# Performance work log

Hardware: AMD Instinct MI355X
Metric: run time of the kernel (lower is better)

The kernel has to match this reference:

```python
import jax, jax.numpy as jnp
import numpy as np

B, T, LA, L = 4, 32, 32, 512
D, H, C = 2048, 16, 128
KV_DIM = 2048
K = T * LA  # total kv tokens per batch element
EPS = 1e-5


def _ln(x):
    m = jnp.mean(x, axis=-1, keepdims=True)
    v = jnp.var(x, axis=-1, keepdims=True)
    return (x - m) * jax.lax.rsqrt(v + EPS)


def setup_inputs() -> dict:
    key = jax.random.key(0)
    ks = jax.random.split(key, 10)
    s = 1.0 / np.sqrt(D)
    sk = 1.0 / np.sqrt(KV_DIM)
    return {
        "x": jax.random.normal(ks[0], (B, T, LA, KV_DIM), jnp.float32),
        "latents": jax.random.normal(ks[1], (B, L, D), jnp.float32),
        "t_emb": jax.random.normal(ks[2], (B, 3, D), jnp.float32) * 0.02,
        "q_lens": jnp.full((B,), L, dtype=jnp.int32),
        "k_lens": jax.random.randint(ks[3], (B,), K // 2, K + 1).astype(jnp.int32),
        "ln_kv_w": jnp.ones((KV_DIM,), jnp.float32),
        "ln_kv_b": jnp.zeros((KV_DIM,), jnp.float32),
        "ssg": jax.random.normal(ks[4], (1, 3, D), jnp.float32) * s,  # shift_scale_gate param (adaLN=True)
        "Wq": jax.random.normal(ks[5], (D, D), jnp.float32) * s,
        "bq": jnp.zeros((D,), jnp.float32),
        "Wkv": jax.random.normal(ks[6], (KV_DIM, 2 * D), jnp.float32) * sk,
        "bkv": jnp.zeros((2 * D,), jnp.float32),
        "Wo": jax.random.normal(ks[7], (D, D), jnp.float32) * s,
        "bo": jnp.zeros((D,), jnp.float32),
    }


def reference(x, latents, t_emb, q_lens, k_lens, ln_kv_w, ln_kv_b, ssg,
              Wq, bq, Wkv, bkv, Wo, bo):
    # norm_kv (affine LayerNorm over kv_dim)
    xk = _ln(x) * ln_kv_w + ln_kv_b  # (B,T,LA,KV_DIM)
    # AdaLN modulate: shift/scale/gate from t_emb + learned shift_scale_gate
    mod = t_emb + ssg  # (B,3,D)
    shift, scale, gate = mod[:, 0:1], mod[:, 1:2], mod[:, 2:3]  # (B,1,D)
    norm_q = _ln(latents)  # norm_q has no affine when adaLN=True
    lat = norm_q * (1.0 + scale) + shift
    # projections
    q = (lat @ Wq + bq).reshape(B, L, H, C)
    kv = (xk.reshape(B, K, KV_DIM) @ Wkv + bkv)  # (B,K,2D)
    k, v = kv[..., :D], kv[..., D:]
    k = k.reshape(B, K, H, C)
    v = v.reshape(B, K, H, C)
    # varlen attention == per-batch masked attention (keys beyond k_lens masked)
    scores = jnp.einsum("blhc,bkhc->bhlk", q, k) / np.sqrt(C)
    kmask = jnp.arange(K)[None, :] < k_lens[:, None]  # (B,K)
    scores = jnp.where(kmask[:, None, None, :], scores, jnp.finfo(scores.dtype).min)
    attn = jax.nn.softmax(scores, axis=-1)
    out = jnp.einsum("bhlk,bkhc->blhc", attn, v).reshape(B, L, D)
    # queries beyond q_lens are invalid -> zero them (varlen packing semantics)
    qmask = (jnp.arange(L)[None, :] < q_lens[:, None])[..., None]  # (B,L,1)
    out = out * qmask
    return (out @ Wo + bo) * gate
```

## Files before the change

kernel.cpp:

```cpp
#include <hip/hip_runtime.h>

typedef unsigned short u16;
typedef short bf16x8 __attribute__((ext_vector_type(8)));
typedef float f32x4 __attribute__((ext_vector_type(4)));

#define MFMA_BF16(a, b, c) __builtin_amdgcn_mfma_f32_16x16x32_bf16((a), (b), (c), 0, 0, 0)

__device__ __forceinline__ u16 f2bf(float f) {
  union { float f; unsigned int u; } cv;
  cv.f = f;
  unsigned int u = cv.u + 0x7fffu + ((cv.u >> 16) & 1u);
  return (u16)(u >> 16);
}

__global__ __launch_bounds__(256) void ln_fused_kernel(
    const float* __restrict__ x, const float* __restrict__ w,
    const float* __restrict__ b, const float* __restrict__ latents,
    const float* __restrict__ t_emb, const float* __restrict__ ssg,
    u16* __restrict__ xk_out, u16* __restrict__ lat_out)
{
  const int blk = blockIdx.x;
  const bool is_x = blk < 4096;
  const int row = is_x ? blk : blk - 4096;
  const int tid = threadIdx.x;
  const float* src = is_x ? (x + (size_t)row * 2048) : (latents + (size_t)row * 2048);
  const float4* xr = (const float4*)src;
  float4 v0 = xr[tid];
  float4 v1 = xr[tid + 256];
  float sum = v0.x + v0.y + v0.z + v0.w + v1.x + v1.y + v1.z + v1.w;
  float sq  = v0.x*v0.x + v0.y*v0.y + v0.z*v0.z + v0.w*v0.w
            + v1.x*v1.x + v1.y*v1.y + v1.z*v1.z + v1.w*v1.w;
  #pragma unroll
  for (int off = 32; off > 0; off >>= 1) {
    sum += __shfl_xor(sum, off);
    sq  += __shfl_xor(sq, off);
  }
  __shared__ float red[8];
  if ((tid & 63) == 0) { red[tid >> 6] = sum; red[(tid >> 6) + 4] = sq; }
  __syncthreads();
  sum = red[0] + red[1] + red[2] + red[3];
  sq  = red[4] + red[5] + red[6] + red[7];
  const float mean = sum * (1.0f / 2048.0f);
  const float var  = sq * (1.0f / 2048.0f) - mean * mean;
  const float rstd = rsqrtf(var + 1e-5f);
  if (is_x) {
    const float4* w4 = (const float4*)w;
    const float4* b4 = (const float4*)b;
    ushort4* orow = (ushort4*)(xk_out + (size_t)row * 2048);
    #pragma unroll
    for (int j = 0; j < 2; ++j) {
      const int idx = tid + j * 256;
      const float4 v = j ? v1 : v0;
      const float4 ww = w4[idx];
      const float4 bb = b4[idx];
      ushort4 o;
      o.x = f2bf((v.x - mean) * rstd * ww.x + bb.x);
      o.y = f2bf((v.y - mean) * rstd * ww.y + bb.y);
      o.z = f2bf((v.z - mean) * rstd * ww.z + bb.z);
      o.w = f2bf((v.w - mean) * rstd * ww.w + bb.w);
      orow[idx] = o;
    }
  } else {
    const int bidx = row >> 9;
    const float4* te = (const float4*)(t_emb + (size_t)bidx * 3 * 2048);
    const float4* sg = (const float4*)ssg;
    ushort4* orow = (ushort4*)(lat_out + (size_t)row * 2048);
    #pragma unroll
    for (int j = 0; j < 2; ++j) {
      const int idx = tid + j * 256;
      const float4 v = j ? v1 : v0;
      const float4 t0 = te[idx];
      const float4 t1 = te[512 + idx];
      const float4 s0 = sg[idx];
      const float4 s1 = sg[512 + idx];
      ushort4 o;
      o.x = f2bf(((v.x - mean) * rstd) * (1.0f + t1.x + s1.x) + (t0.x + s0.x));
      o.y = f2bf(((v.y - mean) * rstd) * (1.0f + t1.y + s1.y) + (t0.y + s0.y));
      o.z = f2bf(((v.z - mean) * rstd) * (1.0f + t1.z + s1.z) + (t0.z + s0.z));
      o.w = f2bf(((v.w - mean) * rstd) * (1.0f + t1.w + s1.w) + (t0.w + s0.w));
      orow[idx] = o;
    }
  }
}

__global__ __launch_bounds__(256) void transpose_all_kernel(
    const float* __restrict__ Wq, const float* __restrict__ Wo,
    const float* __restrict__ Wkv,
    u16* __restrict__ WqT, u16* __restrict__ WoT, u16* __restrict__ WkvT)
{
  __shared__ float tile[32][33];
  int t = blockIdx.x;
  const float* in;
  u16* outp;
  int C, cx, ry;
  if (t < 4096)       { in = Wq;  outp = WqT;  C = 2048; cx = t & 63;  ry = t >> 6; }
  else if (t < 8192)  { t -= 4096; in = Wo;  outp = WoT;  C = 2048; cx = t & 63;  ry = t >> 6; }
  else                { t -= 8192; in = Wkv; outp = WkvT; C = 4096; cx = t & 127; ry = t >> 7; }
  const int R = 2048;
  const int c0 = cx * 32;
  const int r0 = ry * 32;
  const int tx = threadIdx.x & 31;
  const int ty = threadIdx.x >> 5;
  #pragma unroll
  for (int i = 0; i < 4; ++i)
    tile[ty + i * 8][tx] = in[(size_t)(r0 + ty + i * 8) * C + c0 + tx];
  __syncthreads();
  #pragma unroll
  for (int i = 0; i < 4; ++i)
    outp[(size_t)(c0 + ty + i * 8) * R + r0 + tx] = f2bf(tile[tx][ty + i * 8]);
}

template<int BM>
__global__ __launch_bounds__(256) void gemm_bf16_kernel(
    const u16* __restrict__ A, const u16* __restrict__ BT,
    int M, int N, int Kd, int mode,
    const float* __restrict__ bias,
    u16* __restrict__ out_q, u16* __restrict__ out_k, u16* __restrict__ out_vT,
    float* __restrict__ out_f,
    const float* __restrict__ t_emb, const float* __restrict__ ssg)
{
  constexpr int TI = BM / 32;
  __shared__ u16 As[2][BM][40];
  __shared__ u16 Bs[2][128][40];
  const int tid  = threadIdx.x;
  const int lane = tid & 63;
  const int wv   = tid >> 6;
  const int wm   = wv & 1, wn = wv >> 1;
  const int quad = lane >> 4, lq = lane & 15;
  const int m0 = blockIdx.y * BM, n0 = blockIdx.x * 128;

  f32x4 acc[TI][4];
  #pragma unroll
  for (int i = 0; i < TI; ++i)
    #pragma unroll
    for (int j = 0; j < 4; ++j)
      acc[i][j] = (f32x4){0.f, 0.f, 0.f, 0.f};

  const int rB  = tid >> 1;
  const int hfB = (tid & 1) * 16;
  const u16* gB = BT + (size_t)(n0 + rB) * Kd + hfB;
  const int rA  = (BM == 128) ? (tid >> 1) : (tid >> 2);
  const int hA  = (BM == 128) ? 0 : ((tid >> 1) & 1);
  const int hfA = (tid & 1) * 16;
  const u16* gA = A + (size_t)(m0 + rA) * Kd + hA * 32 + hfA;

  for (int k0 = 0; k0 < Kd; k0 += 64) {
    uint4 a00, a01, a10, a11;
    a00 = *(const uint4*)(gA + k0);
    a01 = *(const uint4*)(gA + k0 + 8);
    if (BM == 128) {
      a10 = *(const uint4*)(gA + k0 + 32);
      a11 = *(const uint4*)(gA + k0 + 40);
    }
    const uint4 b00 = *(const uint4*)(gB + k0);
    const uint4 b01 = *(const uint4*)(gB + k0 + 8);
    const uint4 b10 = *(const uint4*)(gB + k0 + 32);
    const uint4 b11 = *(const uint4*)(gB + k0 + 40);
    __syncthreads();
    *(uint4*)&As[hA][rA][hfA]     = a00;
    *(uint4*)&As[hA][rA][hfA + 8] = a01;
    if (BM == 128) {
      *(uint4*)&As[1][rA][hfA]     = a10;
      *(uint4*)&As[1][rA][hfA + 8] = a11;
    }
    *(uint4*)&Bs[0][rB][hfB]     = b00;
    *(uint4*)&Bs[0][rB][hfB + 8] = b01;
    *(uint4*)&Bs[1][rB][hfB]     = b10;
    *(uint4*)&Bs[1][rB][hfB + 8] = b11;
    __syncthreads();
    #pragma unroll
    for (int kk = 0; kk < 2; ++kk) {
      bf16x8 av[TI], bv[4];
      #pragma unroll
      for (int i = 0; i < TI; ++i)
        av[i] = *(const bf16x8*)&As[kk][wm * (BM / 2) + i * 16 + lq][quad * 8];
      #pragma unroll
      for (int j = 0; j < 4; ++j)
        bv[j] = *(const bf16x8*)&Bs[kk][wn * 64 + j * 16 + lq][quad * 8];
      #pragma unroll
      for (int i = 0; i < TI; ++i)
        #pragma unroll
        for (int j = 0; j < 4; ++j)
          acc[i][j] = MFMA_BF16(av[i], bv[j], acc[i][j]);
    }
  }

  #pragma unroll
  for (int i = 0; i < TI; ++i) {
    const int mlb = m0 + wm * (BM / 2) + i * 16 + quad * 4;
    #pragma unroll
    for (int j = 0; j < 4; ++j) {
      const int n = n0 + wn * 64 + j * 16 + lq;
      const float bs = bias[n];
      if (mode == 0) {
        const int h = n >> 7, c = n & 127;
        #pragma unroll
        for (int rr = 0; rr < 4; ++rr) {
          const int m = mlb + rr;
          const int bb = m >> 9, l = m & 511;
          out_q[((size_t)(bb * 16 + h) * 512 + l) * 128 + c] = f2bf(acc[i][j][rr] + bs);
        }
      } else if (mode == 1) {
        if (n < 2048) {
          const int h = n >> 7, c = n & 127;
          #pragma unroll
          for (int rr = 0; rr < 4; ++rr) {
            const int m = mlb + rr;
            const int bb = m >> 10, kk = m & 1023;
            out_k[((size_t)(bb * 16 + h) * 1024 + kk) * 128 + c] = f2bf(acc[i][j][rr] + bs);
          }
        } else {
          const int n2 = n - 2048;
          const int h = n2 >> 7, c = n2 & 127;
          #pragma unroll
          for (int rr = 0; rr < 4; ++rr) {
            const int m = mlb + rr;
            const int bb = m >> 10, kk = m & 1023;
            out_vT[((size_t)(bb * 16 + h) * 128 + c) * 1024 + kk] = f2bf(acc[i][j][rr] + bs);
          }
        }
      } else {
        #pragma unroll
        for (int rr = 0; rr < 4; ++rr) {
          const int m = mlb + rr;
          const int bb = m >> 9;
          const float g = t_emb[((size_t)bb * 3 + 2) * 2048 + n] + ssg[2 * 2048 + n];
          out_f[(size_t)m * 2048 + n] = (acc[i][j][rr] + bs) * g;
        }
      }
    }
  }
}

#define ATT_SCALE 0.08838834764831845f

__global__ __launch_bounds__(256) void attn_kernel(
    const u16* __restrict__ qb, const u16* __restrict__ kb,
    const u16* __restrict__ vT, const int* __restrict__ k_lens,
    const int* __restrict__ q_lens, u16* __restrict__ ao)
{
  __shared__ u16 p_lds[64][72];
  const int tid  = threadIdx.x;
  const int w    = tid >> 6;
  const int lane = tid & 63;
  const int quad = lane >> 4, lq = lane & 15;
  const int bh = blockIdx.y;
  const int b  = bh >> 4;
  const int l0 = blockIdx.x * 64;
  const int kl = k_lens[b];
  const int ql = q_lens[b];

  bf16x8 qf[4];
  {
    const u16* qp = qb + ((size_t)bh * 512 + l0 + w * 16 + lq) * 128 + quad * 8;
    #pragma unroll
    for (int ks = 0; ks < 4; ++ks)
      qf[ks] = *(const bf16x8*)(qp + ks * 32);
  }

  f32x4 o[8];
  #pragma unroll
  for (int j = 0; j < 8; ++j) o[j] = (f32x4){0.f, 0.f, 0.f, 0.f};
  float mrun[4], lrun[4];
  #pragma unroll
  for (int rr = 0; rr < 4; ++rr) { mrun[rr] = -__builtin_inff(); lrun[rr] = 0.f; }

  const int nkt = (kl + 63) >> 6;
  for (int kt = 0; kt < nkt; ++kt) {
    const int k0 = kt * 64;
    f32x4 s[4];
    const u16* kp = kb + ((size_t)bh * 1024 + k0) * 128 + quad * 8;
    #pragma unroll
    for (int ct = 0; ct < 4; ++ct) {
      s[ct] = (f32x4){0.f, 0.f, 0.f, 0.f};
      const u16* kpp = kp + (size_t)(ct * 16 + lq) * 128;
      #pragma unroll
      for (int ks = 0; ks < 4; ++ks) {
        const bf16x8 kf = *(const bf16x8*)(kpp + ks * 32);
        s[ct] = MFMA_BF16(qf[ks], kf, s[ct]);
      }
    }
    #pragma unroll
    for (int ct = 0; ct < 4; ++ct) {
      const bool valid = (k0 + ct * 16 + lq) < kl;
      #pragma unroll
      for (int rr = 0; rr < 4; ++rr) {
        const float sv = s[ct][rr] * ATT_SCALE;
        s[ct][rr] = valid ? sv : -__builtin_inff();
      }
    }
    float mnew[4], alpha[4], rs[4];
    #pragma unroll
    for (int rr = 0; rr < 4; ++rr) {
      float tm = fmaxf(fmaxf(s[0][rr], s[1][rr]), fmaxf(s[2][rr], s[3][rr]));
      tm = fmaxf(tm, __shfl_xor(tm, 1));
      tm = fmaxf(tm, __shfl_xor(tm, 2));
      tm = fmaxf(tm, __shfl_xor(tm, 4));
      tm = fmaxf(tm, __shfl_xor(tm, 8));
      const float mn = fmaxf(mrun[rr], tm);
      alpha[rr] = __expf(mrun[rr] - mn);
      mrun[rr] = mn;
      mnew[rr] = mn;
      rs[rr] = 0.f;
    }
    #pragma unroll
    for (int ct = 0; ct < 4; ++ct)
      #pragma unroll
      for (int rr = 0; rr < 4; ++rr) {
        const float p = __expf(s[ct][rr] - mnew[rr]);
        s[ct][rr] = p;
        rs[rr] += p;
      }
    #pragma unroll
    for (int rr = 0; rr < 4; ++rr) {
      float t = rs[rr];
      t += __shfl_xor(t, 1);
      t += __shfl_xor(t, 2);
      t += __shfl_xor(t, 4);
      t += __shfl_xor(t, 8);
      lrun[rr] = lrun[rr] * alpha[rr] + t;
    }
    #pragma unroll
    for (int j = 0; j < 8; ++j)
      #pragma unroll
      for (int rr = 0; rr < 4; ++rr)
        o[j][rr] *= alpha[rr];

    #pragma unroll
    for (int ct = 0; ct < 4; ++ct)
      #pragma unroll
      for (int rr = 0; rr < 4; ++rr)
        p_lds[w * 16 + quad * 4 + rr][ct * 16 + lq] = f2bf(s[ct][rr]);

    bf16x8 pf[2];
    pf[0] = *(const bf16x8*)&p_lds[w * 16 + lq][quad * 8];
    pf[1] = *(const bf16x8*)&p_lds[w * 16 + lq][32 + quad * 8];

    const u16* vp = vT + (size_t)bh * 128 * 1024 + k0 + quad * 8;
    #pragma unroll
    for (int j = 0; j < 8; ++j) {
      #pragma unroll
      for (int ks2 = 0; ks2 < 2; ++ks2) {
        const bf16x8 vf = *(const bf16x8*)(vp + (size_t)(j * 16 + lq) * 1024 + ks2 * 32);
        o[j] = MFMA_BF16(pf[ks2], vf, o[j]);
      }
    }
  }

  const int h = bh & 15;
  #pragma unroll
  for (int rr = 0; rr < 4; ++rr) {
    const int row = l0 + w * 16 + quad * 4 + rr;
    const float inv = (row < ql) ? (1.0f / lrun[rr]) : 0.0f;
    u16* op = ao + ((size_t)b * 512 + row) * 2048 + h * 128 + lq;
    #pragma unroll
    for (int j = 0; j < 8; ++j)
      op[j * 16] = f2bf(o[j][rr] * inv);
  }
}

extern "C" void kernel_launch(void* const* d_in, const int* in_sizes, int n_in,
                              void* d_out, int out_size, void* d_ws, size_t ws_size,
                              hipStream_t stream) {
  (void)in_sizes; (void)n_in; (void)out_size; (void)ws_size;
  const float* x       = (const float*)d_in[0];
  const float* latents = (const float*)d_in[1];
  const float* t_emb   = (const float*)d_in[2];
  const int*   q_lens  = (const int*)d_in[3];
  const int*   k_lens  = (const int*)d_in[4];
  const float* ln_w    = (const float*)d_in[5];
  const float* ln_b    = (const float*)d_in[6];
  const float* ssg     = (const float*)d_in[7];
  const float* Wq      = (const float*)d_in[8];
  const float* bq      = (const float*)d_in[9];
  const float* Wkv     = (const float*)d_in[10];
  const float* bkv     = (const float*)d_in[11];
  const float* Wo      = (const float*)d_in[12];
  const float* bo      = (const float*)d_in[13];
  float* out = (float*)d_out;

  u16* ws = (u16*)d_ws;
  const size_t MEG = (size_t)1 << 20;
  u16* WqT  = ws;
  u16* WoT  = ws + 4  * MEG;
  u16* WkvT = ws + 8  * MEG;
  u16* xk   = ws + 16 * MEG;
  u16* lat  = ws + 24 * MEG;
  u16* qb   = ws + 28 * MEG;
  u16* kbuf = ws + 32 * MEG;
  u16* vTb  = ws + 40 * MEG;
  u16* aob  = ws + 48 * MEG;

  ln_fused_kernel<<<dim3(6144), dim3(256), 0, stream>>>(
      x, ln_w, ln_b, latents, t_emb, ssg, xk, lat);

  transpose_all_kernel<<<dim3(16384), dim3(256), 0, stream>>>(
      Wq, Wo, Wkv, WqT, WoT, WkvT);

  gemm_bf16_kernel<64><<<dim3(16, 32), dim3(256), 0, stream>>>(
      lat, WqT, 2048, 2048, 2048, 0, bq, qb, nullptr, nullptr, nullptr, nullptr, nullptr);
  gemm_bf16_kernel<128><<<dim3(32, 32), dim3(256), 0, stream>>>(
      xk, WkvT, 4096, 4096, 2048, 1, bkv, nullptr, kbuf, vTb, nullptr, nullptr, nullptr);

  attn_kernel<<<dim3(8, 64), dim3(256), 0, stream>>>(qb, kbuf, vTb, k_lens, q_lens, aob);

  gemm_bf16_kernel<64><<<dim3(16, 32), dim3(256), 0, stream>>>(
      aob, WoT, 2048, 2048, 2048, 2, bo, nullptr, nullptr, nullptr, out, t_emb, ssg);
}
```

Measured before the change: 442.3 us.

## Stage K/V tiles in LDS for attention, fold softmax scale into Q

In the attention kernel, each block now cooperatively loads each 64-key K tile and the matching V^T tile into shared memory with coalesced 16-byte loads. The four waves then share those tiles instead of each wave issuing strided global loads of the same K/V data. The 1/sqrt(C) scale moves into the Q projection epilogue, which removes a multiply per score. The GEMM mode also becomes a template parameter so the epilogue branch is resolved at compile time. The cost is two extra barriers per key tile, more LDS use that may lower occupancy, and Q rounded to bf16 after scaling.

Measured after the change: 432.0 us. 2.3% less time.

```diff
diff --git a/kernel.cpp b/kernel.cpp
--- a/kernel.cpp
+++ b/kernel.cpp
@@ -5,6 +5,7 @@
 typedef float f32x4 __attribute__((ext_vector_type(4)));
 
 #define MFMA_BF16(a, b, c) __builtin_amdgcn_mfma_f32_16x16x32_bf16((a), (b), (c), 0, 0, 0)
+#define ATT_SCALE 0.08838834764831845f
 
 __device__ __forceinline__ u16 f2bf(float f) {
   union { float f; unsigned int u; } cv;
@@ -110,10 +111,10 @@
     outp[(size_t)(c0 + ty + i * 8) * R + r0 + tx] = f2bf(tile[tx][ty + i * 8]);
 }
 
-template<int BM>
+template<int BM, int MODE>
 __global__ __launch_bounds__(256) void gemm_bf16_kernel(
     const u16* __restrict__ A, const u16* __restrict__ BT,
-    int M, int N, int Kd, int mode,
+    int Kd,
     const float* __restrict__ bias,
     u16* __restrict__ out_q, u16* __restrict__ out_k, u16* __restrict__ out_vT,
     float* __restrict__ out_f,
@@ -192,15 +193,16 @@
     for (int j = 0; j < 4; ++j) {
       const int n = n0 + wn * 64 + j * 16 + lq;
       const float bs = bias[n];
-      if (mode == 0) {
+      if (MODE == 0) {
         const int h = n >> 7, c = n & 127;
         #pragma unroll
         for (int rr = 0; rr < 4; ++rr) {
           const int m = mlb + rr;
           const int bb = m >> 9, l = m & 511;
-          out_q[((size_t)(bb * 16 + h) * 512 + l) * 128 + c] = f2bf(acc[i][j][rr] + bs);
+          out_q[((size_t)(bb * 16 + h) * 512 + l) * 128 + c] =
+              f2bf((acc[i][j][rr] + bs) * ATT_SCALE);
         }
-      } else if (mode == 1) {
+      } else if (MODE == 1) {
         if (n < 2048) {
           const int h = n >> 7, c = n & 127;
           #pragma unroll
@@ -232,14 +234,14 @@
   }
 }
 
-#define ATT_SCALE 0.08838834764831845f
-
 __global__ __launch_bounds__(256) void attn_kernel(
     const u16* __restrict__ qb, const u16* __restrict__ kb,
     const u16* __restrict__ vT, const int* __restrict__ k_lens,
     const int* __restrict__ q_lens, u16* __restrict__ ao)
 {
-  __shared__ u16 p_lds[64][72];
+  __shared__ u16 Ks[64][132];
+  __shared__ u16 Vs[128][68];
+  __shared__ u16 Ps[64][68];
   const int tid  = threadIdx.x;
   const int w    = tid >> 6;
   const int lane = tid & 63;
@@ -258,6 +260,13 @@
       qf[ks] = *(const bf16x8*)(qp + ks * 32);
   }
 
+  const int krow = tid >> 4;
+  const int kcol = tid & 15;
+  const u16* kg = kb + ((size_t)bh * 1024 + krow) * 128 + kcol * 8;
+  const int vrow = tid >> 3;
+  const int vcol = tid & 7;
+  const u16* vg = vT + (size_t)bh * 128 * 1024 + (size_t)vrow * 1024 + vcol * 8;
+
   f32x4 o[8];
   #pragma unroll
   for (int j = 0; j < 8; ++j) o[j] = (f32x4){0.f, 0.f, 0.f, 0.f};
@@ -268,15 +277,29 @@
   const int nkt = (kl + 63) >> 6;
   for (int kt = 0; kt < nkt; ++kt) {
     const int k0 = kt * 64;
+    uint4 kd[4], vd[4];
+    #pragma unroll
+    for (int p = 0; p < 4; ++p)
+      kd[p] = *(const uint4*)(kg + (size_t)(k0 + p * 16) * 128);
+    #pragma unroll
+    for (int p = 0; p < 4; ++p)
+      vd[p] = *(const uint4*)(vg + (size_t)p * 32 * 1024 + k0);
+    __syncthreads();
+    #pragma unroll
+    for (int p = 0; p < 4; ++p)
+      *(uint4*)&Ks[krow + p * 16][kcol * 8] = kd[p];
+    #pragma unroll
+    for (int p = 0; p < 4; ++p)
+      *(uint4*)&Vs[vrow + p * 32][vcol * 8] = vd[p];
+    __syncthreads();
+
     f32x4 s[4];
-    const u16* kp = kb + ((size_t)bh * 1024 + k0) * 128 + quad * 8;
     #pragma unroll
     for (int ct = 0; ct < 4; ++ct) {
       s[ct] = (f32x4){0.f, 0.f, 0.f, 0.f};
-      const u16* kpp = kp + (size_t)(ct * 16 + lq) * 128;
       #pragma unroll
       for (int ks = 0; ks < 4; ++ks) {
-        const bf16x8 kf = *(const bf16x8*)(kpp + ks * 32);
+        const bf16x8 kf = *(const bf16x8*)&Ks[ct * 16 + lq][ks * 32 + quad * 8];
         s[ct] = MFMA_BF16(qf[ks], kf, s[ct]);
       }
     }
@@ -284,10 +307,8 @@
     for (int ct = 0; ct < 4; ++ct) {
       const bool valid = (k0 + ct * 16 + lq) < kl;
       #pragma unroll
-      for (int rr = 0; rr < 4; ++rr) {
-        const float sv = s[ct][rr] * ATT_SCALE;
-        s[ct][rr] = valid ? sv : -__builtin_inff();
-      }
+      for (int rr = 0; rr < 4; ++rr)
+        s[ct][rr] = valid ? s[ct][rr] : -__builtin_inff();
     }
     float mnew[4], alpha[4], rs[4];
     #pragma unroll
@@ -330,19 +351,18 @@
     for (int ct = 0; ct < 4; ++ct)
       #pragma unroll
       for (int rr = 0; rr < 4; ++rr)
-        p_lds[w * 16 + quad * 4 + rr][ct * 16 + lq] = f2bf(s[ct][rr]);
+        Ps[w * 16 + quad * 4 + rr][ct * 16 + lq] = f2bf(s[ct][rr]);
 
     bf16x8 pf[2];
-    pf[0] = *(const bf16x8*)&p_lds[w * 16 + lq][quad * 8];
-    pf[1] = *(const bf16x8*)&p_lds[w * 16 + lq][32 + quad * 8];
-
-    const u16* vp = vT + (size_t)bh * 128 * 1024 + k0 + quad * 8;
+    pf[0] = *(const bf16x8*)&Ps[w * 16 + lq][quad * 8];
+    pf[1] = *(const bf16x8*)&Ps[w * 16 + lq][32 + quad * 8];
+
     #pragma unroll
     for (int j = 0; j < 8; ++j) {
       #pragma unroll
-      for (int ks2 = 0; ks2 < 2; ++ks2) {
-        const bf16x8 vf = *(const bf16x8*)(vp + (size_t)(j * 16 + lq) * 1024 + ks2 * 32);
-        o[j] = MFMA_BF16(pf[ks2], vf, o[j]);
+      for (int kk = 0; kk < 2; ++kk) {
+        const bf16x8 vf = *(const bf16x8*)&Vs[j * 16 + lq][kk * 32 + quad * 8];
+        o[j] = MFMA_BF16(pf[kk], vf, o[j]);
       }
     }
   }
@@ -397,13 +417,13 @@
   transpose_all_kernel<<<dim3(16384), dim3(256), 0, stream>>>(
       Wq, Wo, Wkv, WqT, WoT, WkvT);
 
-  gemm_bf16_kernel<64><<<dim3(16, 32), dim3(256), 0, stream>>>(
-      lat, WqT, 2048, 2048, 2048, 0, bq, qb, nullptr, nullptr, nullptr, nullptr, nullptr);
-  gemm_bf16_kernel<128><<<dim3(32, 32), dim3(256), 0, stream>>>(
-      xk, WkvT, 4096, 4096, 2048, 1, bkv, nullptr, kbuf, vTb, nullptr, nullptr, nullptr);
+  gemm_bf16_kernel<64, 0><<<dim3(16, 32), dim3(256), 0, stream>>>(
+      lat, WqT, 2048, bq, qb, nullptr, nullptr, nullptr, nullptr, nullptr);
+  gemm_bf16_kernel<128, 1><<<dim3(32, 32), dim3(256), 0, stream>>>(
+      xk, WkvT, 2048, bkv, nullptr, kbuf, vTb, nullptr, nullptr, nullptr);
 
   attn_kernel<<<dim3(8, 64), dim3(256), 0, stream>>>(qb, kbuf, vTb, k_lens, q_lens, aob);
 
-  gemm_bf16_kernel<64><<<dim3(16, 32), dim3(256), 0, stream>>>(
-      aob, WoT, 2048, 2048, 2048, 2, bo, nullptr, nullptr, nullptr, out, t_emb, ssg);
-}
+  gemm_bf16_kernel<64, 2><<<dim3(16, 32), dim3(256), 0, stream>>>(
+      aob, WoT, 2048, bo, nullptr, nullptr, nullptr, out, t_emb, ssg);
+}
```
